# Optimization experiments

Measured on AMD Instinct MI355X. Metric: run time of the kernel, lower is better.

Reference implementation:

```python
import jax, jax.numpy as jnp
import numpy as np

H = 512          # HIDDEN_DIM
W = 480          # WINDOWWIDTH
NL = 8           # NUMLABELS (output_dim)
STEPS = W // 15  # 32 decoder steps
ATT = W // 16    # 30 attention positions
B = 4            # window batch
L = 12           # per-frame sequence length
D_IN = 32        # input_dim
N = B * W        # 1920 frame sequences


def _lstm(x, Wih, Whh, bih, bhh):
    # x: [T, Bn, Din] -> per-step hidden/cell states [T, Bn, Hd] (torch LSTM gate order i,f,g,o)
    xp = x @ Wih.T + (bih + bhh)
    h0 = jnp.zeros((x.shape[1], Whh.shape[1]), x.dtype)
    def step(carry, xt):
        h, c = carry
        g = xt + h @ Whh.T
        i, f, gg, o = jnp.split(g, 4, axis=-1)
        c = jax.nn.sigmoid(f) * c + jax.nn.sigmoid(i) * jnp.tanh(gg)
        h = jax.nn.sigmoid(o) * jnp.tanh(c)
        return (h, c), (h, c)
    _, (hs, cs) = jax.lax.scan(step, (h0, h0), xp)
    return hs, cs


def _bilstm(x, Wf, Uf, bf, cf, Wb, Ub, bb, cb):
    # x: [Bt, T, D] batch_first; returns ([Bt, T, 2H], h_fwd_final, h_bwd_final)
    xt = jnp.swapaxes(x, 0, 1)
    hf, _ = _lstm(xt, Wf, Uf, bf, cf)
    hb, _ = _lstm(xt[::-1], Wb, Ub, bb, cb)
    out = jnp.concatenate([hf, hb[::-1]], axis=-1)
    return jnp.swapaxes(out, 0, 1), hf[-1], hb[-1]


def _forward(xs, xlengths, enc_Wih, enc_Whh, enc_bih, enc_bhh,
             penc_Wih_f, penc_Whh_f, penc_bih_f, penc_bhh_f,
             penc_Wih_b, penc_Whh_b, penc_bih_b, penc_bhh_b,
             attn_W, attn_b, comb_W, comb_b,
             gru_Wih, gru_Whh, gru_bih, gru_bhh, out_W, out_b):
    # frame-level encoder: packed sequences -> (h, c) at each sequence's true length
    hs, cs = _lstm(xs, enc_Wih, enc_Whh, enc_bih, enc_bhh)   # [L, N, H] each
    idx = xlengths - 1
    ar = jnp.arange(N)
    ctx = jnp.concatenate([hs[idx, ar], cs[idx, ar]], axis=-1)  # [N, 2H]
    ctx = ctx.reshape(B, W // 2, 4 * H)
    # pyramidal BiLSTM stack (dropout is identity at eval)
    out = ctx
    hf = hb = None
    for i in range(4):
        out, hf, hb = _bilstm(ctx, penc_Wih_f[i], penc_Whh_f[i], penc_bih_f[i], penc_bhh_f[i],
                              penc_Wih_b[i], penc_Whh_b[i], penc_bih_b[i], penc_bhh_b[i])
        if i < 3:
            ctx = out.reshape(B, W // (2 ** (i + 2)), 4 * H)
    enc_out = out                                   # [B, ATT, 2H]
    hidden0 = jnp.concatenate([hf, hb], axis=-1)    # [B, 2H]

    def dstep(carry, _):
        inp, h = carry                              # [B, NL], [B, 2H]
        aw = jax.nn.softmax(jnp.concatenate([inp, h], axis=-1) @ attn_W.T + attn_b, axis=-1)
        ctxv = jnp.einsum('bt,btd->bd', aw, enc_out)
        x = jax.nn.relu(jnp.concatenate([inp, ctxv], axis=-1) @ comb_W.T + comb_b)
        # torch GRU cell (gate order r, z, n)
        gi = x @ gru_Wih.T + gru_bih
        gh = h @ gru_Whh.T + gru_bhh
        ir, iz, inn = jnp.split(gi, 3, axis=-1)
        hr, hz, hn = jnp.split(gh, 3, axis=-1)
        r = jax.nn.sigmoid(ir + hr)
        z = jax.nn.sigmoid(iz + hz)
        n = jnp.tanh(inn + r * hn)
        hnew = (1.0 - z) * n + z * h
        logp = jax.nn.log_softmax(hnew @ out_W.T + out_b, axis=-1)
        return (logp, hnew), logp                   # free-running: next input = log-probs

    inp0 = jnp.zeros((B, NL), xs.dtype)
    _, outs = jax.lax.scan(dstep, (inp0, hidden0), None, length=STEPS)  # [STEPS, B, NL]
    return jnp.swapaxes(outs, 0, 1).reshape(B * STEPS, NL)


def setup_inputs() -> dict:
    key = jax.random.key(0)
    ks = jax.random.split(key, 24)
    s = 0.03
    def nrm(k, shape):
        return jax.random.normal(k, shape, dtype=jnp.float32) * s
    return {
        'xs': jax.random.normal(ks[0], (L, N, D_IN), dtype=jnp.float32),
        'xlengths': jax.random.randint(ks[1], (N,), 1, L + 1, dtype=jnp.int32),
        'enc_Wih': nrm(ks[2], (4 * H, D_IN)),
        'enc_Whh': nrm(ks[3], (4 * H, H)),
        'enc_bih': nrm(ks[4], (4 * H,)),
        'enc_bhh': nrm(ks[5], (4 * H,)),
        'penc_Wih_f': nrm(ks[6], (4, 4 * H, 4 * H)),
        'penc_Whh_f': nrm(ks[7], (4, 4 * H, H)),
        'penc_bih_f': nrm(ks[8], (4, 4 * H)),
        'penc_bhh_f': nrm(ks[9], (4, 4 * H)),
        'penc_Wih_b': nrm(ks[10], (4, 4 * H, 4 * H)),
        'penc_Whh_b': nrm(ks[11], (4, 4 * H, H)),
        'penc_bih_b': nrm(ks[12], (4, 4 * H)),
        'penc_bhh_b': nrm(ks[13], (4, 4 * H)),
        'attn_W': nrm(ks[14], (ATT, 2 * H + NL)),
        'attn_b': nrm(ks[15], (ATT,)),
        'comb_W': nrm(ks[16], (H, 2 * H + NL)),
        'comb_b': nrm(ks[17], (H,)),
        'gru_Wih': nrm(ks[18], (3 * 2 * H, H)),
        'gru_Whh': nrm(ks[19], (3 * 2 * H, 2 * H)),
        'gru_bih': nrm(ks[20], (3 * 2 * H,)),
        'gru_bhh': nrm(ks[21], (3 * 2 * H,)),
        'out_W': nrm(ks[22], (NL, 2 * H)),
        'out_b': nrm(ks[23], (NL,)),
    }


def reference(xs, xlengths, enc_Wih, enc_Whh, enc_bih, enc_bhh,
              penc_Wih_f, penc_Whh_f, penc_bih_f, penc_bhh_f,
              penc_Wih_b, penc_Whh_b, penc_bih_b, penc_bhh_b,
              attn_W, attn_b, comb_W, comb_b,
              gru_Wih, gru_Whh, gru_bih, gru_bhh, out_W, out_b):
    return _forward(xs, xlengths, enc_Wih, enc_Whh, enc_bih, enc_bhh,
                    penc_Wih_f, penc_Whh_f, penc_bih_f, penc_bhh_f,
                    penc_Wih_b, penc_Whh_b, penc_bih_b, penc_bhh_b,
                    attn_W, attn_b, comb_W, comb_b,
                    gru_Wih, gru_Whh, gru_bih, gru_bhh, out_W, out_b)
```

## Files before the change

### kernel.cpp

```cpp
#include <hip/hip_runtime.h>
#include <stdint.h>

typedef __attribute__((ext_vector_type(8))) __bf16 bf16x8;
typedef __attribute__((ext_vector_type(4))) float f32x4;
typedef __attribute__((ext_vector_type(4))) unsigned u32x4;

#define DEVI static __device__ __forceinline__
#define SENT 0xFFFFFFFFu

DEVI bf16x8 bzero8(){ bf16x8 r;
#pragma unroll
  for (int i=0;i<8;++i) r[i]=(__bf16)0.0f; return r; }

DEVI bf16x8 ld8(const __bf16* p){ return *(const bf16x8*)p; }
DEVI void st8(__bf16* p, bf16x8 v){ *(bf16x8*)p = v; }

DEVI f32x4 MFMA(bf16x8 a, bf16x8 b, f32x4 c){
  return __builtin_amdgcn_mfma_f32_16x16x32_bf16(a, b, c, 0, 0, 0);
}

DEVI float sigf(float x){ return 1.0f/(1.0f+__expf(-x)); }

DEVI void ast(unsigned* p, unsigned v){ __hip_atomic_store(p, v, __ATOMIC_RELAXED, __HIP_MEMORY_SCOPE_AGENT); }

DEVI unsigned packbf(float a, float b){
  union { __bf16 h[2]; unsigned u; } x; x.h[0]=(__bf16)a; x.h[1]=(__bf16)b; return x.u;
}
DEVI float bflo(unsigned u){ return __builtin_bit_cast(float, u<<16); }
DEVI float bfhi(unsigned u){ return __builtin_bit_cast(float, u & 0xffff0000u); }

DEVI unsigned bad4(u32x4 v){ return (v[0]==SENT)|(v[1]==SENT)|(v[2]==SENT)|(v[3]==SENT); }

DEVI u32x4 ald4(const void* p){
  u32x4 v;
  asm volatile("global_load_dwordx4 %0, %1, off sc0 sc1\n\ts_waitcnt vmcnt(0)"
               : "=&v"(v) : "v"(p) : "memory");
  return v;
}
DEVI u32x4 poll4(const void* p){
  u32x4 v = ald4(p);
  while (bad4(v)){ __builtin_amdgcn_s_sleep(1); v = ald4(p); }
  return v;
}
DEVI void ald4x2(const void* p, u32x4& a, u32x4& b){
  asm volatile("global_load_dwordx4 %0, %2, off sc0 sc1\n\t"
               "global_load_dwordx4 %1, %2, off offset:16 sc0 sc1\n\t"
               "s_waitcnt vmcnt(0)"
               : "=&v"(a), "=&v"(b) : "v"(p) : "memory");
}
DEVI void poll4x2(const void* p, u32x4& a, u32x4& b){
  ald4x2(p, a, b);
  while (bad4(a) | bad4(b)){ __builtin_amdgcn_s_sleep(1); ald4x2(p, a, b); }
}

DEVI void packGroup(const float* W, int Nsrc, int Kreal, int NT, __bf16* dst, long g){
  int kt = (int)(g / (NT*64));
  int rem = (int)(g % (NT*64));
  int nt = rem >> 6, ln = rem & 63;
  int row = nt*16 + (ln & 15);
  int col = kt*32 + ((ln >> 4) << 3);
  bf16x8 v = bzero8();
  if (row < Nsrc){
#pragma unroll
    for (int j=0;j<8;++j){ int c = col + j; if (c < Kreal) v[j] = (__bf16)W[(long)row*Kreal + c]; }
  }
  st8(dst + g*8, v);
}

DEVI void packGroupCat(const float* Wih, const float* Whh, __bf16* dst, long g){
  int kt = (int)(g / (128*64));
  int rem = (int)(g % (128*64));
  int nt = rem >> 6, ln = rem & 63;
  int prow = nt*16 + (ln & 15);
  int src = (prow & 3)*512 + (prow >> 2);
  int col = kt*32 + ((ln >> 4) << 3);
  bf16x8 v;
  if (col < 32){
#pragma unroll
    for (int j=0;j<8;++j) v[j] = (__bf16)Wih[(long)src*32 + col + j];
  } else {
#pragma unroll
    for (int j=0;j<8;++j) v[j] = (__bf16)Whh[(long)src*512 + (col-32) + j];
  }
  st8(dst + g*8, v);
}

__global__ void initK(unsigned* hb){
  int g = blockIdx.x*256 + threadIdx.x;
  if (g < 6144) hb[2048 + g] = SENT;
}

__global__ void packSmallK(const float* __restrict__ xs, const float* __restrict__ eWih,
    const float* __restrict__ eWhh, const float* __restrict__ ebih, const float* __restrict__ ebhh,
    const float* __restrict__ attnW,
    __bf16* __restrict__ xsb, __bf16* __restrict__ wcatp, float* __restrict__ biasc,
    __bf16* __restrict__ attnp)
{
  long g = (long)blockIdx.x*blockDim.x + threadIdx.x;
  const long nWcat = 17L*128*64;
  const long nXs   = 92160;
  const long nBias = 2048;
  const long nAttn = 33L*2*64;
  if (g < nWcat){ packGroupCat(eWih, eWhh, wcatp, g); return; }
  g -= nWcat;
  if (g < nXs){
    const float* s = xs + g*8; bf16x8 v;
#pragma unroll
    for (int j=0;j<8;++j) v[j] = (__bf16)s[j];
    st8(xsb + g*8, v); return;
  }
  g -= nXs;
  if (g < nBias){ int src = ((int)g & 3)*512 + ((int)g >> 2); biasc[g] = ebih[src] + ebhh[src]; return; }
  g -= nBias;
  if (g < nAttn){ packGroup(attnW, 30, 1032, 2, attnp, g); return; }
}

__global__ void packPencK(const float* __restrict__ Wf, const float* __restrict__ Wb,
    const float* __restrict__ WhF, const float* __restrict__ WhB,
    const float* __restrict__ bihf, const float* __restrict__ bhhf,
    const float* __restrict__ bihb, const float* __restrict__ bhhb,
    __bf16* __restrict__ pf, __bf16* __restrict__ pb, float* __restrict__ bsum,
    __bf16* __restrict__ pwhh, unsigned* __restrict__ hpy)
{
  long g = (long)blockIdx.x*blockDim.x + threadIdx.x;
  const long nW = 64L*128*64;
  if (g < nW){ packGroup(Wf, 2048, 2048, 128, pf, g); return; }
  g -= nW;
  if (g < nW){ packGroup(Wb, 2048, 2048, 128, pb, g); return; }
  g -= nW;
  if (g < 2048){ bsum[g] = bihf[g] + bhhf[g]; return; }
  g -= 2048;
  if (g < 2048){ bsum[2048+g] = bihb[g] + bhhb[g]; return; }
  g -= 2048;
  if (g < 8192){
    hpy[g] = ((g >> 10) & 3) ? SENT : 0u;
    return;
  }
  g -= 8192;
  if (g < 262144){
    int lane = (int)(g & 63);
    int f    = (int)((g >> 6) & 31);
    int w    = (int)((g >> 11) & 3);
    int slot = (int)((g >> 13) & 15);
    int dir  = (int)((g >> 17) & 1);
    int kt = f >> 1, nt = f & 1;
    int row16 = lane & 15, kch = lane >> 4;
    int srow = w*512 + slot*32 + nt*16 + row16;
    int scol = kt*32 + kch*8;
    const float* W = dir ? WhB : WhF;
    bf16x8 v;
#pragma unroll
    for (int j=0;j<8;++j) v[j] = (__bf16)W[(long)srow*512 + scol + j];
    st8(pwhh + g*8, v);
  }
}

__global__ __launch_bounds__(256, 1) void encStepK(
    const __bf16* __restrict__ xsb,
    __bf16* __restrict__ henc,
    float* __restrict__ cenc,
    const __bf16* __restrict__ wcatp,
    const float* __restrict__ biasc,
    const int* __restrict__ xlen,
    __bf16* __restrict__ ctx,
    int t)
{
  __shared__ float glds[64][260];
  const int tid = threadIdx.x;
  const int w = tid >> 6, ln = tid & 63;
  const int m0 = blockIdx.x * 64;
  const int nb = blockIdx.y;
  f32x4 acc[16];
#pragma unroll
  for (int i=0;i<16;++i) acc[i] = (f32x4){0.f,0.f,0.f,0.f};

  const int arow = m0 + w*16 + (ln & 15);
  const int kc = (ln >> 4) << 3;
  const int ktEnd = (t == 0) ? 1 : 17;
  for (int kt = 0; kt < ktEnd; ++kt){
    bf16x8 a;
    if (kt == 0) a = ld8(xsb + ((long)t*1920 + arow)*32 + kc);
    else         a = ld8(henc + (long)arow*512 + (kt-1)*32 + kc);
    const __bf16* bp = wcatp + (((long)kt*128 + nb*16)*64 + ln)*8;
#pragma unroll
    for (int n2 = 0; n2 < 16; ++n2){
      bf16x8 b = ld8(bp + (long)n2*512);
      acc[n2] = MFMA(a, b, acc[n2]);
    }
  }
  const int r4 = (ln >> 4) << 2;
#pragma unroll
  for (int n2 = 0; n2 < 16; ++n2){
#pragma unroll
    for (int r = 0; r < 4; ++r)
      glds[w*16 + r4 + r][n2*16 + (ln & 15)] = acc[n2][r];
  }
  __syncthreads();
  for (int it = 0; it < 16; ++it){
    int idx = tid + it*256;
    int mrow = idx >> 6, hcl = idx & 63;
    int n = m0 + mrow;
    int hcg = nb*64 + hcl;
    float ig = glds[mrow][hcl*4+0] + biasc[nb*256 + hcl*4+0];
    float fg = glds[mrow][hcl*4+1] + biasc[nb*256 + hcl*4+1];
    float gg = glds[mrow][hcl*4+2] + biasc[nb*256 + hcl*4+2];
    float og = glds[mrow][hcl*4+3] + biasc[nb*256 + hcl*4+3];
    float c_old = (t == 0) ? 0.0f : cenc[(long)n*512 + hcg];
    float cn = sigf(fg)*c_old + sigf(ig)*tanhf(gg);
    float h  = sigf(og)*tanhf(cn);
    cenc[(long)n*512 + hcg] = cn;
    henc[(long)n*512 + hcg] = (__bf16)h;
    if (xlen[n] - 1 == t){
      ctx[(long)n*1024 + hcg]       = (__bf16)h;
      ctx[(long)n*1024 + 512 + hcg] = (__bf16)cn;
    }
  }
}

__global__ __launch_bounds__(1024) void pencInK(
   const __bf16* __restrict__ inb,
   const __bf16* __restrict__ wpf, const __bf16* __restrict__ wpb,
   const float* __restrict__ bsum,
   float* __restrict__ xpf, float* __restrict__ xpb,
   int M)
{
  const int tid = threadIdx.x, ln = tid & 63, wv = tid >> 6;
  const int rg = wv >> 2, cg = wv & 3;
  const int dir = blockIdx.z;
  const int m0 = blockIdx.x*64 + rg*16;
  const int nb = blockIdx.y;
  const __bf16* wp = dir ? wpb : wpf;
  float* xp = dir ? xpb : xpf;
  const float* bs = bsum + dir*2048;
  f32x4 acc[4];
#pragma unroll
  for (int i=0;i<4;++i) acc[i] = (f32x4){0.f,0.f,0.f,0.f};
  const int arow = m0 + (ln & 15);
  const int kc = (ln >> 4) << 3;
  const bool aok = arow < M;
  for (int kt = 0; kt < 64; ++kt){
    bf16x8 a = aok ? ld8(inb + (long)arow*2048 + kt*32 + kc) : bzero8();
    const __bf16* bp = wp + (((long)kt*128 + nb*16 + cg*4)*64 + ln)*8;
#pragma unroll
    for (int q = 0; q < 4; ++q){
      bf16x8 b = ld8(bp + (long)q*512);
      acc[q] = MFMA(a, b, acc[q]);
    }
  }
  const int r4 = (ln >> 4) << 2;
#pragma unroll
  for (int q = 0; q < 4; ++q){
    int col = (nb*16 + cg*4 + q)*16 + (ln & 15);
#pragma unroll
    for (int r = 0; r < 4; ++r){
      int rowo = m0 + r4 + r;
      if (rowo < M) xp[(long)rowo*2048 + col] = acc[q][r] + bs[col];
    }
  }
}

__global__ __launch_bounds__(256, 1) void pyrRecK(
  const __bf16* __restrict__ pwhh,
  const float* __restrict__ xpf, const float* __restrict__ xpb,
  __bf16* __restrict__ hbuf,
  __bf16* __restrict__ outb,
  float* __restrict__ outf,
  float* __restrict__ h0f, __bf16* __restrict__ h0b,
  int T, int isLast)
{
  __shared__ __align__(16) __bf16 hsL[2][4*512];
  __shared__ float glds[4][4][32];
  const int tid = threadIdx.x, ln = tid & 63, w = tid >> 6;
  const int bk = blockIdx.x;
  const int dir = bk >> 4, slot = bk & 15;
  const int hc0 = slot * 32;
  const float* xp = dir ? xpb : xpf;
  unsigned* hbu = (unsigned*)hbuf;

  bf16x8 BF[32];
  {
    const __bf16* wb = pwhh + ((((size_t)(dir*16 + slot)*4 + w)*32)*64 + ln)*8;
#pragma unroll
    for (int f = 0; f < 32; ++f) BF[f] = ld8(wb + (size_t)f*512);
  }

  const int arow = ln & 15;
  const int kc = (ln >> 4) << 3;
  float cv = 0.0f;
  float x0=0.f,x1=0.f,x2=0.f,x3=0.f;
  if (tid < 128){
    int pos0 = dir ? (T-1) : 0;
    const float* xr = xp + ((size_t)((tid>>5)*T + pos0))*2048 + hc0 + (tid & 31);
    x0 = xr[0]; x1 = xr[512]; x2 = xr[1024]; x3 = xr[1536];
  }

  for (int t = 0; t < T; ++t){
    int cur = t & 3, nxt = (t+1) & 3, clr = (t+2) & 3;
    int pos = dir ? (T-1-t) : t;
    {
      u32x4 v = poll4((const char*)hbuf + (size_t)(dir*4 + cur)*4096 + tid*16);
      ((u32x4*)hsL[t & 1])[tid] = v;
    }
    __syncthreads();
    if (tid < 64){
      int b = tid >> 4, i = tid & 15;
      ast(hbu + ((size_t)(dir*4 + clr)*4 + b)*256 + (hc0 >> 1) + i, SENT);
    }
    const __bf16* hs = hsL[t & 1];
    f32x4 a0 = {0.f,0.f,0.f,0.f}, a1 = a0, a2 = a0, a3 = a0;
#pragma unroll
    for (int kt = 0; kt < 16; kt += 2){
      bf16x8 aA = (arow < 4) ? ld8(hs + arow*512 + kt*32 + kc) : bzero8();
      bf16x8 aB = (arow < 4) ? ld8(hs + arow*512 + (kt+1)*32 + kc) : bzero8();
      a0 = MFMA(aA, BF[kt*2+0], a0);
      a1 = MFMA(aA, BF[kt*2+1], a1);
      a2 = MFMA(aB, BF[kt*2+2], a2);
      a3 = MFMA(aB, BF[kt*2+3], a3);
    }
    a0 += a2; a1 += a3;
    float xn0=0.f,xn1=0.f,xn2=0.f,xn3=0.f;
    if (t+1 < T && tid < 128){
      int pos2 = dir ? (T-2-t) : (t+1);
      const float* xr = xp + ((size_t)((tid>>5)*T + pos2))*2048 + hc0 + (tid & 31);
      xn0 = xr[0]; xn1 = xr[512]; xn2 = xr[1024]; xn3 = xr[1536];
    }
    if (ln < 16){
#pragma unroll
      for (int r=0;r<4;++r){ glds[w][r][ln] = a0[r]; glds[w][r][16+ln] = a1[r]; }
    }
    __syncthreads();
    if (tid < 128){
      int b = tid >> 5, hcl = tid & 31, hcg = hc0 + hcl;
      float ig = glds[0][b][hcl] + x0;
      float fg = glds[1][b][hcl] + x1;
      float gg = glds[2][b][hcl] + x2;
      float og = glds[3][b][hcl] + x3;
      cv = sigf(fg)*cv + sigf(ig)*tanhf(gg);
      float h = sigf(og)*tanhf(cv);
      float hn = __shfl_down(h, 1);
      if (!(hcl & 1))
        ast(hbu + ((size_t)(dir*4 + nxt)*4 + b)*256 + (hcg >> 1), packbf(h, hn));
      if (!isLast){
        outb[((long)(b*T + pos))*1024 + dir*512 + hcg] = (__bf16)h;
      } else {
        outf[((long)(b*T + pos))*1024 + dir*512 + hcg] = h;
        if (t == T-1){
          h0f[b*1024 + dir*512 + hcg] = h;
          h0b[b*1024 + dir*512 + hcg] = (__bf16)h;
        }
      }
    }
    x0=xn0; x1=xn1; x2=xn2; x3=xn3;
  }
}

__global__ __launch_bounds__(256) void precMK(const float* __restrict__ combW,
    const float* __restrict__ encOut, __bf16* __restrict__ Mb)
{
  __shared__ float eo[1024];
  int bt = blockIdx.x;
  int b = bt / 30, t = bt % 30;
  int tid = threadIdx.x;
  for (int i = tid; i < 1024; i += 256) eo[i] = encOut[((long)b*30 + t)*1024 + i];
  __syncthreads();
#pragma unroll 1
  for (int cc = 0; cc < 2; ++cc){
    int c = tid*2 + cc;
    const f32x4* wr4 = (const f32x4*)(combW + (long)c*1032 + 8);
    float s = 0.f;
    for (int d = 0; d < 256; ++d){
      f32x4 wv = wr4[d];
      s += wv[0]*eo[d*4] + wv[1]*eo[d*4+1] + wv[2]*eo[d*4+2] + wv[3]*eo[d*4+3];
    }
    Mb[((long)b*30 + t)*512 + c] = (__bf16)s;
  }
}

DEVI bf16x8 dfrag(const __bf16* base, const __bf16* inp, int row, int kt, int kc, int stride){
  if (row >= 4) return bzero8();
  int k = kt*32 + kc;
  if (k == 0) return ld8(inp + row*8);
  int off = k - 8;
  return (off < 1024) ? ld8(base + row*stride + off) : bzero8();
}

__global__ __launch_bounds__(256, 1) void decoderK(
  const float* __restrict__ gWih,
  const float* __restrict__ gWhh,
  const float* __restrict__ gbih, const float* __restrict__ gbhh,
  const float* __restrict__ combW,
  const float* __restrict__ combBias,
  const float* __restrict__ attnBias,
  const float* __restrict__ outW, const float* __restrict__ outBias,
  const __bf16* __restrict__ attnP,
  const __bf16* __restrict__ Mb,
  const float* __restrict__ h0f,
  __bf16* __restrict__ HB,
  float* __restrict__ dout)
{
  __shared__ __align__(16) __bf16 giL[96*512];
  __shared__ __align__(16) __bf16 outWL[8*1024];
  __shared__ __align__(16) __bf16 hL[4*1024];
  __shared__ __align__(16) __bf16 xL[4][520];
  __shared__ __align__(16) __bf16 WcIL[512][8];
  __shared__ __align__(16) __bf16 inpL[32];
  __shared__ float awL[4][32];
  __shared__ float redL[4][8];
  __shared__ float ghL[3][4][32];
  __shared__ float giO[3][4][32];
  __shared__ float biL[3][32], bhL[3][32];
  __shared__ float abL[30];
  __shared__ float cbAllL[512];

  const int tid = threadIdx.x, ln = tid & 63, w = tid >> 6;
  const int slot = blockIdx.x;
  const int hc0 = slot * 32;
  unsigned* HBu = (unsigned*)HB;

  for (int it = 0; it < 24; ++it){
    int g = it*256 + tid;
    int rho = g >> 6, c8 = g & 63;
    int gate = rho >> 5, r = rho & 31;
    const float* s = gWih + ((long)(gate*1024 + hc0 + r))*512 + c8*8;
    bf16x8 v;
#pragma unroll
    for (int j=0;j<8;++j) v[j] = (__bf16)s[j];
    st8((__bf16*)((char*)giL + ((rho*1024 + c8*16) ^ ((rho & 7) << 4))), v);
  }
  for (int it = 0; it < 32; ++it){
    int g = it*256 + tid;
    outWL[g] = (__bf16)outW[g];
  }
  for (int idx = tid; idx < 4096; idx += 256){
    int c = idx >> 3, j = idx & 7;
    WcIL[c][j] = (__bf16)combW[(long)c*1032 + j];
  }
  for (int idx = tid; idx < 512; idx += 256) cbAllL[idx] = combBias[idx];
  if (tid < 96){
    int g2 = tid >> 5, l = tid & 31;
    biL[g2][l] = gbih[g2*1024 + hc0 + l];
    bhL[g2][l] = gbhh[g2*1024 + hc0 + l];
  }
  if (tid < 30) abL[tid] = attnBias[tid];

  const int row = ln & 15, kc = (ln >> 4) << 3;
  bf16x8 bigF[66];
  if (w == 0){
#pragma unroll
    for (int nt = 0; nt < 2; ++nt)
#pragma unroll
      for (int kt = 0; kt < 33; ++kt)
        bigF[nt*33 + kt] = ld8(attnP + (((size_t)kt*2 + nt)*64 + ln)*8);
  } else {
    int gate = w - 1;
#pragma unroll
    for (int nt = 0; nt < 2; ++nt)
#pragma unroll
      for (int kt = 0; kt < 32; ++kt){
        const float* s = gWhh + ((long)(gate*1024 + hc0 + nt*16 + row))*1024 + kt*32 + kc;
        bf16x8 v;
#pragma unroll
        for (int j=0;j<8;++j) v[j] = (__bf16)s[j];
        bigF[nt*33 + kt] = v;
      }
  }

  float hold = 0.f;
  if (tid < 128) hold = h0f[(tid>>5)*1024 + hc0 + (tid & 31)];
  __syncthreads();

  for (int s = 0; s <= 32; ++s){
    int cur = s & 3, nxt = (s+1) & 3, clr = (s+2) & 3;
    {
      u32x4 q0, q1;
      poll4x2((const char*)HB + (size_t)cur*8192 + tid*32, q0, q1);
      ((u32x4*)hL)[tid*2]   = q0;
      ((u32x4*)hL)[tid*2+1] = q1;
    }
    __syncthreads();
    if (tid < 64){
      int b = tid >> 4, i = tid & 15;
      ast(HBu + ((size_t)clr*4 + b)*512 + (hc0 >> 1) + i, SENT);
    }
    if (s == 0){
      if (tid < 32) inpL[tid] = (__bf16)0.0f;
      __syncthreads();
    } else {
      int o = tid >> 3, sl = tid & 7;
      int b = o >> 3, l = o & 7;
      const unsigned* hlp = (const unsigned*)hL + b*512 + sl*64;
      const unsigned* wlp = (const unsigned*)outWL + l*512 + sl*64;
      float p = 0.f;
      for (int kk = 0; kk < 64; ++kk){
        unsigned u = hlp[kk], t2 = wlp[kk];
        p += bflo(u)*bflo(t2) + bfhi(u)*bfhi(t2);
      }
      p += __shfl_down(p, 4);
      p += __shfl_down(p, 2);
      p += __shfl_down(p, 1);
      if (sl == 0) redL[b][l] = p + outBias[l];
      __syncthreads();
      if (tid < 4){
        float m = redL[tid][0];
        for (int l2=1;l2<8;++l2) m = fmaxf(m, redL[tid][l2]);
        float sum = 0.f;
        for (int l2=0;l2<8;++l2) sum += __expf(redL[tid][l2]-m);
        float lse = m + __logf(sum);
        for (int l2=0;l2<8;++l2){
          float lp = redL[tid][l2] - lse;
          inpL[tid*8 + l2] = (__bf16)lp;
          if (slot == 0) dout[((long)tid*32 + (s-1))*8 + l2] = lp;
        }
      }
      __syncthreads();
    }
    if (s == 32) break;

    if (w == 0){
      f32x4 a0 = {0.f,0.f,0.f,0.f}, a1 = {0.f,0.f,0.f,0.f};
#pragma unroll
      for (int kt = 0; kt < 33; ++kt){
        bf16x8 a = dfrag(hL, inpL, row, kt, kc, 1024);
        a0 = MFMA(a, bigF[kt], a0);
        a1 = MFMA(a, bigF[33+kt], a1);
      }
      if (ln < 16){
#pragma unroll
        for (int r=0;r<4;++r) awL[r][ln] = a0[r] + abL[ln];
        if (16 + ln < 30){
#pragma unroll
          for (int r=0;r<4;++r) awL[r][16+ln] = a1[r] + abL[16+ln];
        }
      }
    } else {
      f32x4 a0 = {0.f,0.f,0.f,0.f}, a1 = {0.f,0.f,0.f,0.f};
#pragma unroll
      for (int kt = 0; kt < 32; ++kt){
        int k = kt*32 + kc;
        bf16x8 a = (row < 4) ? ld8(hL + row*1024 + k) : bzero8();
        a0 = MFMA(a, bigF[kt], a0);
        a1 = MFMA(a, bigF[33+kt], a1);
      }
      if (ln < 16){
        int gate = w - 1;
#pragma unroll
        for (int r=0;r<4;++r){
          ghL[gate][r][ln] = a0[r];
          ghL[gate][r][16+ln] = a1[r];
        }
      }
    }
    __syncthreads();
    if (tid < 4){
      float m = awL[tid][0];
      for (int t2=1;t2<30;++t2) m = fmaxf(m, awL[tid][t2]);
      float sum = 0.f;
      for (int t2=0;t2<30;++t2){ float e = __expf(awL[tid][t2]-m); awL[tid][t2] = e; sum += e; }
      float inv = 1.0f/sum;
      for (int t2=0;t2<30;++t2) awL[tid][t2] *= inv;
    }
    __syncthreads();
    {
      int c0 = tid*2;
#pragma unroll 1
      for (int b = 0; b < 4; ++b){
        float z0 = cbAllL[c0], z1 = cbAllL[c0+1];
#pragma unroll
        for (int j = 0; j < 8; ++j){
          float ij = (float)inpL[b*8 + j];
          z0 += (float)WcIL[c0][j]*ij;
          z1 += (float)WcIL[c0+1][j]*ij;
        }
        const unsigned* mp = (const unsigned*)Mb + (((long)b*30)*512 + c0)/2;
#pragma unroll
        for (int t2 = 0; t2 < 30; ++t2){
          unsigned u = mp[t2*256];
          float a = awL[b][t2];
          z0 += a*bflo(u);
          z1 += a*bfhi(u);
        }
        xL[b][c0]   = (__bf16)fmaxf(z0, 0.f);
        xL[b][c0+1] = (__bf16)fmaxf(z1, 0.f);
      }
    }
    __syncthreads();
    if (w >= 1){
      int gate = w - 1;
      f32x4 a0 = {0.f,0.f,0.f,0.f}, a1 = {0.f,0.f,0.f,0.f};
#pragma unroll
      for (int kt = 0; kt < 16; ++kt){
        int k = kt*32 + kc;
        bf16x8 a = (row < 4) ? ld8(&xL[row][k]) : bzero8();
        int r0 = gate*32 + row, r1 = r0 + 16;
        bf16x8 b0 = ld8((__bf16*)((char*)giL + ((r0*1024 + k*2) ^ ((r0 & 7) << 4))));
        bf16x8 b1 = ld8((__bf16*)((char*)giL + ((r1*1024 + k*2) ^ ((r1 & 7) << 4))));
        a0 = MFMA(a, b0, a0);
        a1 = MFMA(a, b1, a1);
      }
      if (ln < 16){
#pragma unroll
        for (int r=0;r<4;++r){
          giO[gate][r][ln] = a0[r] + biL[gate][ln];
          giO[gate][r][16+ln] = a1[r] + biL[gate][16+ln];
        }
      }
    }
    __syncthreads();
    if (tid < 128){
      int b = tid >> 5, l = tid & 31, hcg = hc0 + l;
      float rr = sigf(giO[0][b][l] + ghL[0][b][l] + bhL[0][l]);
      float zz = sigf(giO[1][b][l] + ghL[1][b][l] + bhL[1][l]);
      float nn = tanhf(giO[2][b][l] + rr*(ghL[2][b][l] + bhL[2][l]));
      float hnew = (1.0f - zz)*nn + zz*hold;
      hold = hnew;
      float h2 = __shfl_down(hnew, 1);
      if (!(l & 1))
        ast(HBu + ((size_t)nxt*4 + b)*512 + (hcg >> 1), packbf(hnew, h2));
    }
  }
}

static const size_t O_XSB   = 12288;
static const size_t O_WCATP = 1486848;
static const size_t O_BIASC = 3715072;
static const size_t O_HENC  = 3723264;
static const size_t O_PWHH  = 3723264;
static const size_t O_CENC  = 5689344;
static const size_t O_CTX   = 9621504;
static const size_t O_WIHPF = 13553664;
static const size_t O_WIHPB = 21942272;
static const size_t O_BSUM  = 30330880;
static const size_t O_XPF   = 30347264;
static const size_t O_XPB   = 38211584;
static const size_t O_HPYR  = 46075904;
static const size_t O_OUTA  = 46108672;
static const size_t O_OUTB  = 48074752;
static const size_t O_ENCO  = 49057792;
static const size_t O_H0F   = 49549312;
static const size_t O_HB    = 49565696;
static const size_t O_ATTNP = 49647616;
static const size_t O_M     = 49782784;

extern "C" void kernel_launch(void* const* d_in, const int* in_sizes, int n_in,
                              void* d_out, int out_size, void* d_ws, size_t ws_size,
                              hipStream_t stream)
{
  const float* xs    = (const float*)d_in[0];
  const int*   xlen  = (const int*)d_in[1];
  const float* eWih  = (const float*)d_in[2];
  const float* eWhh  = (const float*)d_in[3];
  const float* ebih  = (const float*)d_in[4];
  const float* ebhh  = (const float*)d_in[5];
  const float* pWihF = (const float*)d_in[6];
  const float* pWhhF = (const float*)d_in[7];
  const float* pbihF = (const float*)d_in[8];
  const float* pbhhF = (const float*)d_in[9];
  const float* pWihB = (const float*)d_in[10];
  const float* pWhhB = (const float*)d_in[11];
  const float* pbihB = (const float*)d_in[12];
  const float* pbhhB = (const float*)d_in[13];
  const float* attnW = (const float*)d_in[14];
  const float* attnb = (const float*)d_in[15];
  const float* combW = (const float*)d_in[16];
  const float* combb = (const float*)d_in[17];
  const float* gWih  = (const float*)d_in[18];
  const float* gWhh  = (const float*)d_in[19];
  const float* gbih  = (const float*)d_in[20];
  const float* gbhh  = (const float*)d_in[21];
  const float* outW  = (const float*)d_in[22];
  const float* outb  = (const float*)d_in[23];

  char* ws = (char*)d_ws;
  __bf16* XSB     = (__bf16*)(ws + O_XSB);
  __bf16* WCATP   = (__bf16*)(ws + O_WCATP);
  float*  BIASC   = (float*)(ws + O_BIASC);
  __bf16* HENC    = (__bf16*)(ws + O_HENC);
  __bf16* PWHH    = (__bf16*)(ws + O_PWHH);
  float*  CENC    = (float*)(ws + O_CENC);
  __bf16* CTX     = (__bf16*)(ws + O_CTX);
  __bf16* WIHPF   = (__bf16*)(ws + O_WIHPF);
  __bf16* WIHPB   = (__bf16*)(ws + O_WIHPB);
  float*  BSUM    = (float*)(ws + O_BSUM);
  float*  XPF     = (float*)(ws + O_XPF);
  float*  XPB     = (float*)(ws + O_XPB);
  __bf16* HPYR    = (__bf16*)(ws + O_HPYR);
  __bf16* OUTA    = (__bf16*)(ws + O_OUTA);
  __bf16* OUTB    = (__bf16*)(ws + O_OUTB);
  float*  ENCO    = (float*)(ws + O_ENCO);
  float*  H0F     = (float*)(ws + O_H0F);
  __bf16* HB      = (__bf16*)(ws + O_HB);
  __bf16* ATTNP   = (__bf16*)(ws + O_ATTNP);
  __bf16* MB      = (__bf16*)(ws + O_M);

  initK<<<24, 256, 0, stream>>>((unsigned*)HB);
  packSmallK<<<929, 256, 0, stream>>>(xs, eWih, eWhh, ebih, ebhh, attnW,
      XSB, WCATP, BIASC, ATTNP);

  for (int t = 0; t < 12; ++t)
    encStepK<<<dim3(30, 8), 256, 0, stream>>>(XSB, HENC, CENC, WCATP, BIASC, xlen, CTX, t);

  const int Ts[4] = {240, 120, 60, 30};
  const __bf16* ins[4] = {CTX, OUTA, OUTB, OUTA};
  __bf16* outs[4] = {OUTA, OUTB, OUTA, OUTB};
  for (int L = 0; L < 4; ++L){
    int T = Ts[L];
    packPencK<<<5168, 256, 0, stream>>>(pWihF + (long)L*2048*2048, pWihB + (long)L*2048*2048,
        pWhhF + (long)L*2048*512, pWhhB + (long)L*2048*512,
        pbihF + L*2048, pbhhF + L*2048, pbihB + L*2048, pbhhB + L*2048,
        WIHPF, WIHPB, BSUM, PWHH, (unsigned*)HPYR);
    int MBk = (4*T + 63)/64;
    pencInK<<<dim3(MBk, 8, 2), 1024, 0, stream>>>(ins[L], WIHPF, WIHPB, BSUM, XPF, XPB, 4*T);
    pyrRecK<<<32, 256, 0, stream>>>(PWHH, XPF, XPB, HPYR, outs[L], ENCO, H0F, HB,
        T, (L==3) ? 1 : 0);
  }

  precMK<<<120, 256, 0, stream>>>(combW, ENCO, MB);

  decoderK<<<32, 256, 0, stream>>>(gWih, gWhh, gbih, gbhh, combW, combb, attnb,
      outW, outb, ATTNP, MB, H0F, HB, (float*)d_out);
}
```

Baseline: 2.211 ms.

## Overlap next-layer weight packing with pyramid recurrence and pad LDS rows

```diff
diff --git a/kernel.cpp b/kernel.cpp
--- a/kernel.cpp
+++ b/kernel.cpp
@@ -22,6 +22,7 @@
 DEVI float sigf(float x){ return 1.0f/(1.0f+__expf(-x)); }
 
 DEVI void ast(unsigned* p, unsigned v){ __hip_atomic_store(p, v, __ATOMIC_RELAXED, __HIP_MEMORY_SCOPE_AGENT); }
+DEVI unsigned ald1(const unsigned* p){ return __hip_atomic_load(p, __ATOMIC_RELAXED, __HIP_MEMORY_SCOPE_AGENT); }
 
 DEVI unsigned packbf(float a, float b){
   union { __bf16 h[2]; unsigned u; } x; x.h[0]=(__bf16)a; x.h[1]=(__bf16)b; return x.u;
@@ -51,6 +52,18 @@
 DEVI void poll4x2(const void* p, u32x4& a, u32x4& b){
   ald4x2(p, a, b);
   while (bad4(a) | bad4(b)){ __builtin_amdgcn_s_sleep(1); ald4x2(p, a, b); }
+}
+
+DEVI void drainvm(){ asm volatile("s_waitcnt vmcnt(0)" ::: "memory"); }
+
+DEVI void flagbar(unsigned* slots, int nblk, int bk, unsigned ep){
+  __syncthreads();
+  if (threadIdx.x == 0) ast(slots + (size_t)bk*16, ep);
+  if ((int)threadIdx.x < nblk){
+    const unsigned* sp = slots + (size_t)threadIdx.x*16;
+    while (ald1(sp) < ep) __builtin_amdgcn_s_sleep(1);
+  }
+  __syncthreads();
 }
 
 DEVI void packGroup(const float* W, int Nsrc, int Kreal, int NT, __bf16* dst, long g){
@@ -85,44 +98,12 @@
   st8(dst + g*8, v);
 }
 
-__global__ void initK(unsigned* hb){
-  int g = blockIdx.x*256 + threadIdx.x;
-  if (g < 6144) hb[2048 + g] = SENT;
-}
-
-__global__ void packSmallK(const float* __restrict__ xs, const float* __restrict__ eWih,
-    const float* __restrict__ eWhh, const float* __restrict__ ebih, const float* __restrict__ ebhh,
-    const float* __restrict__ attnW,
-    __bf16* __restrict__ xsb, __bf16* __restrict__ wcatp, float* __restrict__ biasc,
-    __bf16* __restrict__ attnp)
-{
-  long g = (long)blockIdx.x*blockDim.x + threadIdx.x;
-  const long nWcat = 17L*128*64;
-  const long nXs   = 92160;
-  const long nBias = 2048;
-  const long nAttn = 33L*2*64;
-  if (g < nWcat){ packGroupCat(eWih, eWhh, wcatp, g); return; }
-  g -= nWcat;
-  if (g < nXs){
-    const float* s = xs + g*8; bf16x8 v;
-#pragma unroll
-    for (int j=0;j<8;++j) v[j] = (__bf16)s[j];
-    st8(xsb + g*8, v); return;
-  }
-  g -= nXs;
-  if (g < nBias){ int src = ((int)g & 3)*512 + ((int)g >> 2); biasc[g] = ebih[src] + ebhh[src]; return; }
-  g -= nBias;
-  if (g < nAttn){ packGroup(attnW, 30, 1032, 2, attnp, g); return; }
-}
-
-__global__ void packPencK(const float* __restrict__ Wf, const float* __restrict__ Wb,
-    const float* __restrict__ WhF, const float* __restrict__ WhB,
-    const float* __restrict__ bihf, const float* __restrict__ bhhf,
-    const float* __restrict__ bihb, const float* __restrict__ bhhb,
-    __bf16* __restrict__ pf, __bf16* __restrict__ pb, float* __restrict__ bsum,
-    __bf16* __restrict__ pwhh, unsigned* __restrict__ hpy)
-{
-  long g = (long)blockIdx.x*blockDim.x + threadIdx.x;
+#define NPACKITEMS 1314816L
+DEVI void packPencItem(long g,
+    const float* Wf, const float* Wb, const float* WhF, const float* WhB,
+    const float* bihf, const float* bhhf, const float* bihb, const float* bhhb,
+    __bf16* pf, __bf16* pb, float* bsum, __bf16* pwhh)
+{
   const long nW = 64L*128*64;
   if (g < nW){ packGroup(Wf, 2048, 2048, 128, pf, g); return; }
   g -= nW;
@@ -132,11 +113,6 @@
   g -= 2048;
   if (g < 2048){ bsum[2048+g] = bihb[g] + bhhb[g]; return; }
   g -= 2048;
-  if (g < 8192){
-    hpy[g] = ((g >> 10) & 3) ? SENT : 0u;
-    return;
-  }
-  g -= 8192;
   if (g < 262144){
     int lane = (int)(g & 63);
     int f    = (int)((g >> 6) & 31);
@@ -153,6 +129,55 @@
     for (int j=0;j<8;++j) v[j] = (__bf16)W[(long)srow*512 + scol + j];
     st8(pwhh + g*8, v);
   }
+}
+
+__global__ void initK(unsigned* bar, unsigned* hb){
+  int g = blockIdx.x*256 + threadIdx.x;
+  if (g < 3072){ bar[g] = 0u; return; }
+  g -= 3072;
+  if (g < 6144){ hb[2048 + g] = SENT; return; }
+}
+
+__global__ void packSmallK(const float* __restrict__ xs, const float* __restrict__ eWih,
+    const float* __restrict__ eWhh, const float* __restrict__ ebih, const float* __restrict__ ebhh,
+    const float* __restrict__ attnW,
+    __bf16* __restrict__ xsb, __bf16* __restrict__ wcatp, float* __restrict__ biasc,
+    __bf16* __restrict__ attnp)
+{
+  long g = (long)blockIdx.x*blockDim.x + threadIdx.x;
+  const long nWcat = 17L*128*64;
+  const long nXs   = 92160;
+  const long nBias = 2048;
+  const long nAttn = 33L*2*64;
+  if (g < nWcat){ packGroupCat(eWih, eWhh, wcatp, g); return; }
+  g -= nWcat;
+  if (g < nXs){
+    const float* s = xs + g*8; bf16x8 v;
+#pragma unroll
+    for (int j=0;j<8;++j) v[j] = (__bf16)s[j];
+    st8(xsb + g*8, v); return;
+  }
+  g -= nXs;
+  if (g < nBias){ int src = ((int)g & 3)*512 + ((int)g >> 2); biasc[g] = ebih[src] + ebhh[src]; return; }
+  g -= nBias;
+  if (g < nAttn){ packGroup(attnW, 30, 1032, 2, attnp, g); return; }
+}
+
+__global__ void packPencK(const float* __restrict__ Wf, const float* __restrict__ Wb,
+    const float* __restrict__ WhF, const float* __restrict__ WhB,
+    const float* __restrict__ bihf, const float* __restrict__ bhhf,
+    const float* __restrict__ bihb, const float* __restrict__ bhhb,
+    __bf16* __restrict__ pf, __bf16* __restrict__ pb, float* __restrict__ bsum,
+    __bf16* __restrict__ pwhh, unsigned* __restrict__ hpy)
+{
+  long g = (long)blockIdx.x*blockDim.x + threadIdx.x;
+  if (g < 8192){
+    hpy[g] = ((g >> 10) & 3) ? SENT : 0u;
+    return;
+  }
+  g -= 8192;
+  if (g < NPACKITEMS)
+    packPencItem(g, Wf, Wb, WhF, WhB, bihf, bhhf, bihb, bhhb, pf, pb, bsum, pwhh);
 }
 
 __global__ __launch_bounds__(256, 1) void encStepK(
@@ -266,12 +291,30 @@
   __bf16* __restrict__ outb,
   float* __restrict__ outf,
   float* __restrict__ h0f, __bf16* __restrict__ h0b,
-  int T, int isLast)
-{
-  __shared__ __align__(16) __bf16 hsL[2][4*512];
+  int T, int isLast, int L, int hasPack,
+  const float* __restrict__ nWf, const float* __restrict__ nWb,
+  const float* __restrict__ nWhF, const float* __restrict__ nWhB,
+  const float* __restrict__ nbihf, const float* __restrict__ nbhhf,
+  const float* __restrict__ nbihb, const float* __restrict__ nbhhb,
+  __bf16* __restrict__ pf2, __bf16* __restrict__ pb2,
+  float* __restrict__ bsum2, __bf16* __restrict__ pwhh2,
+  unsigned* __restrict__ cnt, unsigned* __restrict__ slotsBase)
+{
+  __shared__ __align__(16) __bf16 hsL[2][4*528];
   __shared__ float glds[4][4][32];
   const int tid = threadIdx.x, ln = tid & 63, w = tid >> 6;
   const int bk = blockIdx.x;
+
+  if (bk >= 32){
+    if (!hasPack) return;
+    if (tid == 0){ while (ald1(cnt) < 32u) __builtin_amdgcn_s_sleep(2); }
+    __syncthreads();
+    long g = (long)(bk - 32)*256 + tid;
+    if (g < NPACKITEMS)
+      packPencItem(g, nWf, nWb, nWhF, nWhB, nbihf, nbhhf, nbihb, nbhhb, pf2, pb2, bsum2, pwhh2);
+    return;
+  }
+
   const int dir = bk >> 4, slot = bk & 15;
   const int hc0 = slot * 32;
   const float* xp = dir ? xpb : xpf;
@@ -283,6 +326,18 @@
 #pragma unroll
     for (int f = 0; f < 32; ++f) BF[f] = ld8(wb + (size_t)f*512);
   }
+  drainvm();
+  __syncthreads();
+  if (tid == 0)
+    __hip_atomic_fetch_add(cnt, 1u, __ATOMIC_RELAXED, __HIP_MEMORY_SCOPE_AGENT);
+  if (tid < 64){
+    int b = tid >> 4, i = tid & 15;
+#pragma unroll
+    for (int bu = 0; bu < 4; ++bu)
+      ast(hbu + ((size_t)(dir*4 + bu)*4 + b)*256 + (hc0 >> 1) + i, bu == 0 ? 0u : SENT);
+  }
+  flagbar(slotsBase + dir*256, 16, slot, (unsigned)(L+1));
+  __builtin_amdgcn_s_setprio(1);
 
   const int arow = ln & 15;
   const int kc = (ln >> 4) << 3;
@@ -299,7 +354,8 @@
     int pos = dir ? (T-1-t) : t;
     {
       u32x4 v = poll4((const char*)hbuf + (size_t)(dir*4 + cur)*4096 + tid*16);
-      ((u32x4*)hsL[t & 1])[tid] = v;
+      int e0 = tid*8, r = e0 >> 9, o = e0 & 511;
+      *(u32x4*)(hsL[t & 1] + r*528 + o) = v;
     }
     __syncthreads();
     if (tid < 64){
@@ -310,8 +366,8 @@
     f32x4 a0 = {0.f,0.f,0.f,0.f}, a1 = a0, a2 = a0, a3 = a0;
 #pragma unroll
     for (int kt = 0; kt < 16; kt += 2){
-      bf16x8 aA = (arow < 4) ? ld8(hs + arow*512 + kt*32 + kc) : bzero8();
-      bf16x8 aB = (arow < 4) ? ld8(hs + arow*512 + (kt+1)*32 + kc) : bzero8();
+      bf16x8 aA = (arow < 4) ? ld8(hs + arow*528 + kt*32 + kc) : bzero8();
+      bf16x8 aB = (arow < 4) ? ld8(hs + arow*528 + (kt+1)*32 + kc) : bzero8();
       a0 = MFMA(aA, BF[kt*2+0], a0);
       a1 = MFMA(aA, BF[kt*2+1], a1);
       a2 = MFMA(aB, BF[kt*2+2], a2);
@@ -399,10 +455,10 @@
   float* __restrict__ dout)
 {
   __shared__ __align__(16) __bf16 giL[96*512];
-  __shared__ __align__(16) __bf16 outWL[8*1024];
-  __shared__ __align__(16) __bf16 hL[4*1024];
-  __shared__ __align__(16) __bf16 xL[4][520];
-  __shared__ __align__(16) __bf16 WcIL[512][8];
+  __shared__ __align__(16) __bf16 outWL[8*1040];
+  __shared__ __align__(16) __bf16 hL[4*1040];
+  __shared__ __align__(16) __bf16 xL[4][528];
+  __shared__ __align__(16) __bf16 WcIT[8][520];
   __shared__ __align__(16) __bf16 inpL[32];
   __shared__ float awL[4][32];
   __shared__ float redL[4][8];
@@ -429,11 +485,12 @@
   }
   for (int it = 0; it < 32; ++it){
     int g = it*256 + tid;
-    outWL[g] = (__bf16)outW[g];
+    int r = g >> 10, c = g & 1023;
+    outWL[r*1040 + c] = (__bf16)outW[g];
   }
   for (int idx = tid; idx < 4096; idx += 256){
     int c = idx >> 3, j = idx & 7;
-    WcIL[c][j] = (__bf16)combW[(long)c*1032 + j];
+    WcIT[j][c] = (__bf16)combW[(long)c*1032 + j];
   }
   for (int idx = tid; idx < 512; idx += 256) cbAllL[idx] = combBias[idx];
   if (tid < 96){
@@ -474,8 +531,9 @@
     {
       u32x4 q0, q1;
       poll4x2((const char*)HB + (size_t)cur*8192 + tid*32, q0, q1);
-      ((u32x4*)hL)[tid*2]   = q0;
-      ((u32x4*)hL)[tid*2+1] = q1;
+      int e0 = tid*16, r0 = e0 >> 10, o0 = e0 & 1023;
+      u32x4* d = (u32x4*)(hL + r0*1040 + o0);
+      d[0] = q0; d[1] = q1;
     }
     __syncthreads();
     if (tid < 64){
@@ -488,11 +546,12 @@
     } else {
       int o = tid >> 3, sl = tid & 7;
       int b = o >> 3, l = o & 7;
-      const unsigned* hlp = (const unsigned*)hL + b*512 + sl*64;
-      const unsigned* wlp = (const unsigned*)outWL + l*512 + sl*64;
+      const unsigned* hrow = (const unsigned*)hL + b*520;
+      const unsigned* wrow = (const unsigned*)outWL + l*520;
       float p = 0.f;
-      for (int kk = 0; kk < 64; ++kk){
-        unsigned u = hlp[kk], t2 = wlp[kk];
+#pragma unroll 8
+      for (int j = 0; j < 64; ++j){
+        unsigned u = hrow[sl + 8*j], t2 = wrow[sl + 8*j];
         p += bflo(u)*bflo(t2) + bfhi(u)*bfhi(t2);
       }
       p += __shfl_down(p, 4);
@@ -520,7 +579,7 @@
       f32x4 a0 = {0.f,0.f,0.f,0.f}, a1 = {0.f,0.f,0.f,0.f};
 #pragma unroll
       for (int kt = 0; kt < 33; ++kt){
-        bf16x8 a = dfrag(hL, inpL, row, kt, kc, 1024);
+        bf16x8 a = dfrag(hL, inpL, row, kt, kc, 1040);
         a0 = MFMA(a, bigF[kt], a0);
         a1 = MFMA(a, bigF[33+kt], a1);
       }
@@ -537,7 +596,7 @@
 #pragma unroll
       for (int kt = 0; kt < 32; ++kt){
         int k = kt*32 + kc;
-        bf16x8 a = (row < 4) ? ld8(hL + row*1024 + k) : bzero8();
+        bf16x8 a = (row < 4) ? ld8(hL + row*1040 + k) : bzero8();
         a0 = MFMA(a, bigF[kt], a0);
         a1 = MFMA(a, bigF[33+kt], a1);
       }
@@ -568,8 +627,8 @@
 #pragma unroll
         for (int j = 0; j < 8; ++j){
           float ij = (float)inpL[b*8 + j];
-          z0 += (float)WcIL[c0][j]*ij;
-          z1 += (float)WcIL[c0+1][j]*ij;
+          z0 += (float)WcIT[j][c0]*ij;
+          z1 += (float)WcIT[j][c0+1]*ij;
         }
         const unsigned* mp = (const unsigned*)Mb + (((long)b*30)*512 + c0)/2;
 #pragma unroll
@@ -620,6 +679,7 @@
   }
 }
 
+static const size_t O_BAR   = 0;
 static const size_t O_XSB   = 12288;
 static const size_t O_WCATP = 1486848;
 static const size_t O_BIASC = 3715072;
@@ -639,7 +699,7 @@
 static const size_t O_H0F   = 49549312;
 static const size_t O_HB    = 49565696;
 static const size_t O_ATTNP = 49647616;
-static const size_t O_M     = 49782784;
+static const size_t O_M     = 49715200;
 
 extern "C" void kernel_launch(void* const* d_in, const int* in_sizes, int n_in,
                               void* d_out, int out_size, void* d_ws, size_t ws_size,
@@ -671,6 +731,7 @@
   const float* outb  = (const float*)d_in[23];
 
   char* ws = (char*)d_ws;
+  unsigned* BARU  = (unsigned*)(ws + O_BAR);
   __bf16* XSB     = (__bf16*)(ws + O_XSB);
   __bf16* WCATP   = (__bf16*)(ws + O_WCATP);
   float*  BIASC   = (float*)(ws + O_BIASC);
@@ -692,26 +753,30 @@
   __bf16* ATTNP   = (__bf16*)(ws + O_ATTNP);
   __bf16* MB      = (__bf16*)(ws + O_M);
 
-  initK<<<24, 256, 0, stream>>>((unsigned*)HB);
+  initK<<<36, 256, 0, stream>>>(BARU, (unsigned*)HB);
   packSmallK<<<929, 256, 0, stream>>>(xs, eWih, eWhh, ebih, ebhh, attnW,
       XSB, WCATP, BIASC, ATTNP);
 
   for (int t = 0; t < 12; ++t)
     encStepK<<<dim3(30, 8), 256, 0, stream>>>(XSB, HENC, CENC, WCATP, BIASC, xlen, CTX, t);
+
+  packPencK<<<5168, 256, 0, stream>>>(pWihF, pWihB, pWhhF, pWhhB,
+      pbihF, pbhhF, pbihB, pbhhB, WIHPF, WIHPB, BSUM, PWHH, (unsigned*)HPYR);
 
   const int Ts[4] = {240, 120, 60, 30};
   const __bf16* ins[4] = {CTX, OUTA, OUTB, OUTA};
   __bf16* outs[4] = {OUTA, OUTB, OUTA, OUTB};
   for (int L = 0; L < 4; ++L){
     int T = Ts[L];
-    packPencK<<<5168, 256, 0, stream>>>(pWihF + (long)L*2048*2048, pWihB + (long)L*2048*2048,
-        pWhhF + (long)L*2048*512, pWhhB + (long)L*2048*512,
-        pbihF + L*2048, pbhhF + L*2048, pbihB + L*2048, pbhhB + L*2048,
-        WIHPF, WIHPB, BSUM, PWHH, (unsigned*)HPYR);
     int MBk = (4*T + 63)/64;
     pencInK<<<dim3(MBk, 8, 2), 1024, 0, stream>>>(ins[L], WIHPF, WIHPB, BSUM, XPF, XPB, 4*T);
-    pyrRecK<<<32, 256, 0, stream>>>(PWHH, XPF, XPB, HPYR, outs[L], ENCO, H0F, HB,
-        T, (L==3) ? 1 : 0);
+    int Ln = (L < 3) ? (L+1) : L;
+    pyrRecK<<<(L < 3) ? 5168 : 32, 256, 0, stream>>>(PWHH, XPF, XPB, HPYR,
+        outs[L], ENCO, H0F, HB, T, (L==3) ? 1 : 0, L, (L < 3) ? 1 : 0,
+        pWihF + (long)Ln*2048*2048, pWihB + (long)Ln*2048*2048,
+        pWhhF + (long)Ln*2048*512,  pWhhB + (long)Ln*2048*512,
+        pbihF + Ln*2048, pbhhF + Ln*2048, pbihB + Ln*2048, pbhhB + Ln*2048,
+        WIHPF, WIHPB, BSUM, PWHH, BARU + 512 + L, BARU);
   }
 
   precMK<<<120, 256, 0, stream>>>(combW, ENCO, MB);
```

Result: no change. 2.208 ms (-0.1%).
